# Kernel optimization log

Measured on AMD Instinct MI355X. Metric: run time of the kernel, lower is better.

Reference implementation:

```python
import jax, jax.numpy as jnp
import numpy as np

D_MODEL, N_HEAD, D_HEAD, D_ROPE = 2048, 16, 128, 64
D_KV, D_Q = 512, 1024
THETA = 10000.0


def _cos_sin(seq_len):
    # freqs_cis equivalent: angles [seq_len, d_rope//2]
    inv = 1.0 / (THETA ** (jnp.arange(0, D_ROPE, 2, dtype=jnp.float32) / D_ROPE))
    ang = jnp.arange(seq_len, dtype=jnp.float32)[:, None] * inv[None, :]
    return jnp.cos(ang), jnp.sin(ang)


def _rope(t, cos, sin):
    # t: [b, s, h, d_rope]; rotate interleaved (even, odd) pairs as complex mult
    t1, t2 = t[..., 0::2], t[..., 1::2]
    c = cos[None, :, None, :]
    s = sin[None, :, None, :]
    out = jnp.stack([t1 * c - t2 * s, t1 * s + t2 * c], axis=-1)
    return out.reshape(t.shape)


def setup_inputs() -> dict:
    key = jax.random.key(0)
    ks = jax.random.split(key, 10)
    b, s = 1, 2048
    x = jax.random.normal(ks[0], (b, s, D_MODEL), dtype=jnp.float32)
    # additive causal mask [s, s]
    mask = jnp.where(jnp.tril(jnp.ones((s, s), dtype=bool)), 0.0, -1e9).astype(jnp.float32)
    def w(k, fan_in, fan_out):
        lim = (6.0 / (fan_in + fan_out)) ** 0.5  # xavier_uniform
        return jax.random.uniform(k, (fan_in, fan_out), jnp.float32, -lim, lim)
    return {
        'x': x, 'mask': mask,
        'W_kv_down': w(ks[1], D_MODEL, D_KV),
        'W_k_up':    w(ks[2], D_KV, N_HEAD * D_HEAD),
        'W_v_up':    w(ks[3], D_KV, N_HEAD * D_HEAD),
        'W_q_down':  w(ks[4], D_MODEL, D_Q),
        'W_q_up':    w(ks[5], D_Q, N_HEAD * D_HEAD),
        'W_q_rope':  w(ks[6], D_Q, N_HEAD * D_ROPE),
        'W_k_rope':  w(ks[7], D_MODEL, N_HEAD * D_ROPE),
        'W_out':     w(ks[8], N_HEAD * D_HEAD, D_MODEL),
    }


def reference(x, mask, W_kv_down, W_k_up, W_v_up, W_q_down, W_q_up, W_q_rope, W_k_rope, W_out):
    b, s, _ = x.shape
    cos, sin = _cos_sin(s)
    # low-rank KV path
    down_kv = x @ W_kv_down                                      # [b,s,d_kv]
    k_c = (down_kv @ W_k_up).reshape(b, s, N_HEAD, D_HEAD)
    v   = (down_kv @ W_v_up).reshape(b, s, N_HEAD, D_HEAD)
    # low-rank Q path
    down_q = x @ W_q_down                                        # [b,s,d_q]
    q_c = (down_q @ W_q_up).reshape(b, s, N_HEAD, D_HEAD)
    q_r = (down_q @ W_q_rope).reshape(b, s, N_HEAD, D_ROPE)
    k_r = (x @ W_k_rope).reshape(b, s, N_HEAD, D_ROPE)
    # decoupled RoPE on rope parts only
    q_r = _rope(q_r, cos, sin)
    k_r = _rope(k_r, cos, sin)
    # concat content + rope, heads to dim 1
    q = jnp.concatenate([q_c, q_r], axis=-1).transpose(0, 2, 1, 3)  # [b,h,s,dh+dr]
    k = jnp.concatenate([k_c, k_r], axis=-1).transpose(0, 2, 1, 3)
    vv = v.transpose(0, 2, 1, 3)                                     # [b,h,s,dh]
    scale = 1.0 / jnp.sqrt(jnp.float32(D_HEAD + D_ROPE))
    scores = jnp.einsum('bhqd,bhkd->bhqk', q, k) * scale + mask[None, None]
    probs = jax.nn.softmax(scores.astype(jnp.float32), axis=-1).astype(q.dtype)
    out = jnp.einsum('bhqk,bhkd->bhqd', probs, vv)                   # [b,h,s,dh]
    out = out.transpose(0, 2, 1, 3).reshape(b, s, N_HEAD * D_HEAD)
    return out @ W_out
```

## Files before the change

kernel.cpp:

```cpp
#include <hip/hip_runtime.h>
#include <hip/hip_bf16.h>
#include <math.h>

#define S 2048
#define DM 2048
#define NH 16
#define DH 128
#define DR 64
#define DKV 512
#define DQ 1024
#define DQK 192
#define QSCALE 0.07216878364870323f

typedef __bf16 bf16x8 __attribute__((ext_vector_type(8)));
typedef float f32x4 __attribute__((ext_vector_type(4)));
typedef unsigned short u16;

__device__ inline unsigned int pack2_bf16(float a, float b) {
    __hip_bfloat16 ha = __float2bfloat16(a);
    __hip_bfloat16 hb = __float2bfloat16(b);
    unsigned short ua = *reinterpret_cast<unsigned short*>(&ha);
    unsigned short ub = *reinterpret_cast<unsigned short*>(&hb);
    return (unsigned int)ua | ((unsigned int)ub << 16);
}
__device__ inline u16 f2bf(float v) {
    __hip_bfloat16 hb = __float2bfloat16(v);
    return *reinterpret_cast<u16*>(&hb);
}
__device__ inline void gload_lds16(const void* g, void* l) {
    __builtin_amdgcn_global_load_lds(
        (const __attribute__((address_space(1))) void*)g,
        (__attribute__((address_space(3))) void*)l, 16, 0, 0);
}

__global__ __launch_bounds__(256) void prep_kernel(
    const float* __restrict__ x,
    const float* __restrict__ W0, const float* __restrict__ W1, const float* __restrict__ W2,
    const float* __restrict__ W3, const float* __restrict__ W4, const float* __restrict__ W5,
    const float* __restrict__ W6, const float* __restrict__ W7,
    u16* __restrict__ x_bf,
    u16* __restrict__ D0, u16* __restrict__ D1, u16* __restrict__ D2, u16* __restrict__ D3,
    u16* __restrict__ D4, u16* __restrict__ D5, u16* __restrict__ D6, u16* __restrict__ D7,
    float* __restrict__ cosT, float* __restrict__ sinT) {
    __shared__ u16 tile[64][65];
    const int b = blockIdx.x;
    if (b < 3584) {
        const float* W; u16* D; int N, K, local;
        if (b < 256)       { W = W0; D = D0; N = 512;  K = 2048; local = b; }
        else if (b < 768)  { W = W1; D = D1; N = 1024; K = 2048; local = b - 256; }
        else if (b < 1280) { W = W2; D = D2; N = 1024; K = 2048; local = b - 768; }
        else if (b < 1536) { W = W3; D = D3; N = 2048; K = 512;  local = b - 1280; }
        else if (b < 1792) { W = W4; D = D4; N = 2048; K = 512;  local = b - 1536; }
        else if (b < 2304) { W = W5; D = D5; N = 2048; K = 1024; local = b - 1792; }
        else if (b < 2560) { W = W6; D = D6; N = 1024; K = 1024; local = b - 2304; }
        else               { W = W7; D = D7; N = 2048; K = 2048; local = b - 2560; }
        const int nt = N / 64;
        const int n0 = (local % nt) * 64;
        const int k0 = (local / nt) * 64;
        const int tx = threadIdx.x & 15;
        const int ty = threadIdx.x >> 4;
#pragma unroll
        for (int rep = 0; rep < 4; ++rep) {
            int kk = rep * 16 + ty;
            float4 v = *reinterpret_cast<const float4*>(&W[(size_t)(k0 + kk) * N + n0 + tx * 4]);
            tile[kk][tx * 4 + 0] = f2bf(v.x);
            tile[kk][tx * 4 + 1] = f2bf(v.y);
            tile[kk][tx * 4 + 2] = f2bf(v.z);
            tile[kk][tx * 4 + 3] = f2bf(v.w);
        }
        __syncthreads();
#pragma unroll
        for (int rep = 0; rep < 4; ++rep) {
            int nn = rep * 16 + ty;
            uint2 w;
            w.x = (unsigned int)tile[tx * 4 + 0][nn] | ((unsigned int)tile[tx * 4 + 1][nn] << 16);
            w.y = (unsigned int)tile[tx * 4 + 2][nn] | ((unsigned int)tile[tx * 4 + 3][nn] << 16);
            *reinterpret_cast<uint2*>(&D[(size_t)(n0 + nn) * K + k0 + tx * 4]) = w;
        }
    } else if (b < 7680) {
        int idx = (b - 3584) * 256 + threadIdx.x;
        float4 v = *reinterpret_cast<const float4*>(&x[(size_t)idx * 4]);
        uint2 w;
        w.x = pack2_bf16(v.x, v.y);
        w.y = pack2_bf16(v.z, v.w);
        *reinterpret_cast<uint2*>(&x_bf[(size_t)idx * 4]) = w;
    } else {
        int idx = (b - 7680) * 256 + threadIdx.x;
        int pos = idx / (DR / 2);
        int j   = idx % (DR / 2);
        float inv = __expf(-((float)(2 * j) / (float)DR) * logf(10000.0f));
        float ang = (float)pos * inv;
        cosT[idx] = cosf(ang);
        sinT[idx] = sinf(ang);
    }
}

template <int MODE>
__device__ __forceinline__ void gemm_core(
    u16 (*lds)[6144],
    const u16* __restrict__ A, const u16* __restrict__ BT,
    void* __restrict__ P0v, void* __restrict__ P1v, void* __restrict__ P2v,
    const float* __restrict__ cosT, const float* __restrict__ sinT, int K,
    int bm, int bn) {
    const int tid  = threadIdx.x;
    const int wave = tid >> 6;
    const int lane = tid & 63;
    const int c16  = lane & 15;
    const int g    = lane >> 4;
    const int wm = (wave >> 1) * 32;
    const int wn = (wave & 1) * 64;

    f32x4 acc[2][4];
#pragma unroll
    for (int i = 0; i < 2; ++i)
#pragma unroll
        for (int j = 0; j < 4; ++j) acc[i][j] = f32x4{0.f, 0.f, 0.f, 0.f};

    auto stage = [&](int buf, int k0) {
        {
            int L = tid;
            int rp = L >> 3, e = L & 7, x = e ^ (rp & 7);
            int row = 2 * rp + (x >> 2), kc = x & 3;
            gload_lds16(A + (size_t)(bm + row) * K + k0 + kc * 8, &lds[buf][wave * 512]);
        }
#pragma unroll
        for (int r = 0; r < 2; ++r) {
            int L = r * 256 + tid;
            int rp = L >> 3, e = L & 7, x = e ^ (rp & 7);
            int row = 2 * rp + (x >> 2), kc = x & 3;
            gload_lds16(BT + (size_t)(bn + row) * K + k0 + kc * 8,
                        &lds[buf][2048 + (r * 256 + wave * 64) * 8]);
        }
    };

    const int NT = K / 32;
    stage(0, 0);
    __syncthreads();
    int cur = 0;
    for (int t = 0; t < NT; ++t) {
        if (t + 1 < NT) stage(cur ^ 1, (t + 1) * 32);
        bf16x8 af[2], bfr[4];
#pragma unroll
        for (int i = 0; i < 2; ++i) {
            int row  = wm + i * 16 + c16;
            int slot = ((row >> 1) << 3) + ((((row & 1) << 2) + g) ^ ((row >> 1) & 7));
            af[i] = *reinterpret_cast<const bf16x8*>(&lds[cur][slot * 8]);
        }
#pragma unroll
        for (int j = 0; j < 4; ++j) {
            int row  = wn + j * 16 + c16;
            int slot = ((row >> 1) << 3) + ((((row & 1) << 2) + g) ^ ((row >> 1) & 7));
            bfr[j] = *reinterpret_cast<const bf16x8*>(&lds[cur][2048 + slot * 8]);
        }
#pragma unroll
        for (int i = 0; i < 2; ++i)
#pragma unroll
            for (int j = 0; j < 4; ++j)
                acc[i][j] = __builtin_amdgcn_mfma_f32_16x16x32_bf16(af[i], bfr[j], acc[i][j], 0, 0, 0);
        __syncthreads();
        cur ^= 1;
    }

#pragma unroll
    for (int i = 0; i < 2; ++i)
#pragma unroll
        for (int j = 0; j < 4; ++j) {
            const int mrow = bm + wm + i * 16 + g * 4;
            const int col  = bn + wn + j * 16 + c16;
            if constexpr (MODE == 0) {
                if (col < 512) {
                    u16* down_kv = (u16*)P0v;
#pragma unroll
                    for (int r = 0; r < 4; ++r)
                        down_kv[(size_t)(mrow + r) * DKV + col] = f2bf(acc[i][j][r]);
                } else if (col < 1536) {
                    u16* down_q = (u16*)P1v;
#pragma unroll
                    for (int r = 0; r < 4; ++r)
                        down_q[(size_t)(mrow + r) * DQ + (col - 512)] = f2bf(acc[i][j][r]);
                } else {
                    u16* k_asm = (u16*)P2v;
                    const int cc = col - 1536, h = cc >> 6, rr = cc & 63, jj = rr >> 1;
#pragma unroll
                    for (int r = 0; r < 4; ++r) {
                        int pos = mrow + r;
                        float self = acc[i][j][r];
                        float vp   = __shfl_xor(self, 1);
                        float c = cosT[pos * (DR / 2) + jj];
                        float s = sinT[pos * (DR / 2) + jj];
                        float val = (rr & 1) ? (vp * s + self * c) : (self * c - vp * s);
                        k_asm[((size_t)h * S + pos) * DQK + DH + rr] = f2bf(val);
                    }
                }
            } else if constexpr (MODE == 1) {
                if (col < 2048) {
                    u16* k_asm = (u16*)P0v;
                    const int h = col >> 7, d = col & 127;
#pragma unroll
                    for (int r = 0; r < 4; ++r)
                        k_asm[((size_t)h * S + mrow + r) * DQK + d] = f2bf(acc[i][j][r]);
                } else {
                    u16* vt = (u16*)P1v;
                    const int cc = col - 2048, h = cc >> 7, d = cc & 127;
                    uint2 w;
                    w.x = pack2_bf16(acc[i][j][0], acc[i][j][1]);
                    w.y = pack2_bf16(acc[i][j][2], acc[i][j][3]);
                    *reinterpret_cast<uint2*>(&vt[((size_t)h * DH + d) * S + mrow]) = w;
                }
            } else if constexpr (MODE == 2) {
                u16* q_asm = (u16*)P0v;
                if (col < 2048) {
                    const int h = col >> 7, d = col & 127;
#pragma unroll
                    for (int r = 0; r < 4; ++r)
                        q_asm[((size_t)h * S + mrow + r) * DQK + d] = f2bf(acc[i][j][r] * QSCALE);
                } else {
                    const int cc = col - 2048, h = cc >> 6, rr = cc & 63, jj = rr >> 1;
#pragma unroll
                    for (int r = 0; r < 4; ++r) {
                        int pos = mrow + r;
                        float self = acc[i][j][r];
                        float vp   = __shfl_xor(self, 1);
                        float c = cosT[pos * (DR / 2) + jj];
                        float s = sinT[pos * (DR / 2) + jj];
                        float val = (rr & 1) ? (vp * s + self * c) : (self * c - vp * s);
                        q_asm[((size_t)h * S + pos) * DQK + DH + rr] = f2bf(val * QSCALE);
                    }
                }
            } else {
                float* outp = (float*)P0v;
#pragma unroll
                for (int r = 0; r < 4; ++r)
                    outp[(size_t)(mrow + r) * DM + col] = acc[i][j][r];
            }
        }
}

template <int MODE>
__global__ __launch_bounds__(256) void gemm_fused_kernel(
    const u16* __restrict__ A, const u16* __restrict__ BT,
    void* __restrict__ P0v, void* __restrict__ P1v, void* __restrict__ P2v,
    const float* __restrict__ cosT, const float* __restrict__ sinT, int K) {
    __shared__ u16 lds[2][6144];
    gemm_core<MODE>(lds, A, BT, P0v, P1v, P2v, cosT, sinT, K,
                    blockIdx.y * 64, blockIdx.x * 128);
}

__global__ __launch_bounds__(256) void gemm_g23_kernel(
    const u16* __restrict__ down_kv, const u16* __restrict__ WT2,
    const u16* __restrict__ down_q,  const u16* __restrict__ WT3,
    u16* __restrict__ k_asm, u16* __restrict__ vt, u16* __restrict__ q_asm,
    const float* __restrict__ cosT, const float* __restrict__ sinT) {
    __shared__ u16 lds[2][6144];
    const int b = blockIdx.x;
    if (b < 1024) {
        gemm_core<1>(lds, down_kv, WT2, k_asm, vt, nullptr, cosT, sinT, DKV,
                     (b >> 5) * 64, (b & 31) * 128);
    } else {
        const int l = b - 1024;
        gemm_core<2>(lds, down_q, WT3, q_asm, nullptr, nullptr, cosT, sinT, DQ,
                     (l / 24) * 64, (l % 24) * 128);
    }
}

__global__ __launch_bounds__(512) void attn_mfma_kernel(const u16* __restrict__ q,
                                                        const u16* __restrict__ k,
                                                        const u16* __restrict__ vt,
                                                        u16* __restrict__ outp) {
    const int wgid = blockIdx.x;
    const int xcd  = wgid & 7;
    const int i    = wgid >> 3;
    const int h    = xcd * 2 + (i & 1);
    const int pr   = i >> 1;
    const int qtA  = 31 - pr;
    const int qtB  = pr;

    const int tid  = threadIdx.x;
    const int wave = tid >> 6;
    const int grp  = wave >> 2;
    const int w4   = wave & 3;
    const int lane = tid & 63;
    const int col  = lane & 15;
    const int g    = lane >> 4;

    __shared__ __align__(16) char arena[92160];
    u16* KtG = (u16*)(arena + (grp ? 24576 : 0));
    u16* VtG = (u16*)(arena + 49152 + (grp ? 16384 : 0));
    u16* p_my = (u16*)(arena + 81920 + wave * 1024);
    float2* ml = (float2*)(arena + 90112);
    f32x4* cmb = (f32x4*)(arena);

    const int r7  = col & 7;
    const int pv7 = (col >> 1) & 7;
    const int pvb = (col & 1) << 2;

    auto stage_pair = [&](int buf, int j0E) {
#pragma unroll
        for (int c = 0; c < 5; ++c) {
            int idx = wave + c * 8;
            if (idx < 12) {
                int L = idx * 64 + lane;
                int row = L / 24, rem = L - row * 24;
                int ch  = ((rem >> 3) << 3) + ((rem & 7) ^ (row & 7));
                gload_lds16(k + ((size_t)h * S + j0E + row) * DQK + ch * 8,
                            (u16*)(arena) + buf * 6144 + idx * 512);
            } else if (idx < 20) {
                int s2 = idx - 12;
                int L = s2 * 64 + lane;
                int rp = L >> 3, x = (L & 7) ^ (rp & 7);
                int d  = 2 * rp + (x >> 2), kc = x & 3;
                gload_lds16(vt + ((size_t)h * DH + d) * S + j0E + kc * 8,
                            (u16*)(arena + 49152) + buf * 4096 + s2 * 512);
            } else if (idx < 32) {
                int s2 = idx - 20;
                int L = s2 * 64 + lane;
                int row = L / 24, rem = L - row * 24;
                int ch  = ((rem >> 3) << 3) + ((rem & 7) ^ (row & 7));
                gload_lds16(k + ((size_t)h * S + j0E + 32 + row) * DQK + ch * 8,
                            (u16*)(arena + 24576) + buf * 6144 + s2 * 512);
            } else {
                int s2 = idx - 32;
                int L = s2 * 64 + lane;
                int rp = L >> 3, x = (L & 7) ^ (rp & 7);
                int d  = 2 * rp + (x >> 2), kc = x & 3;
                gload_lds16(vt + ((size_t)h * DH + d) * S + j0E + 32 + kc * 8,
                            (u16*)(arena + 65536) + buf * 4096 + s2 * 512);
            }
        }
    };

    auto phase = [&](int qt) {
        const int q0 = qt * 64;
        const int qw = q0 + w4 * 16;
        const int I  = qt + 1;

        bf16x8 qf[6];
        const u16* qbase = q + ((size_t)h * S + qw + col) * DQK + g * 8;
#pragma unroll
        for (int c = 0; c < 6; ++c) qf[c] = *reinterpret_cast<const bf16x8*>(qbase + c * 32);

        f32x4 acc[8];
#pragma unroll
        for (int c = 0; c < 8; ++c) acc[c] = f32x4{0.f, 0.f, 0.f, 0.f};
        float m_run = -1e30f, l_run = 0.f;

        stage_pair(0, 0);
        __syncthreads();
        for (int tp = 0; tp < I; ++tp) {
            if (tp + 1 < I) stage_pair((tp + 1) & 1, (tp + 1) * 64);
            const int buf = tp & 1;
            const int j0  = tp * 64 + grp * 32;
            const u16* Kc = KtG + buf * 6144;
            const u16* Vc = VtG + buf * 4096;

            f32x4 st[2];
            st[0] = f32x4{0.f, 0.f, 0.f, 0.f};
            st[1] = f32x4{0.f, 0.f, 0.f, 0.f};
#pragma unroll
            for (int tt = 0; tt < 2; ++tt) {
                int rb = (16 * tt + col) * 24;
#pragma unroll
                for (int c = 0; c < 6; ++c) {
                    int ch   = g + 4 * c;
                    int slot = rb + ((ch >> 3) << 3) + ((ch & 7) ^ r7);
                    bf16x8 kf = *reinterpret_cast<const bf16x8*>(Kc + slot * 8);
                    st[tt] = __builtin_amdgcn_mfma_f32_16x16x32_bf16(kf, qf[c], st[tt], 0, 0, 0);
                }
            }
#pragma unroll
            for (int tt = 0; tt < 2; ++tt) {
                if (j0 + 16 * tt + 15 > qw) {
#pragma unroll
                    for (int r = 0; r < 4; ++r) {
                        int key = j0 + 16 * tt + 4 * g + r;
                        st[tt][r] = (key > qw + col) ? -1e30f : st[tt][r];
                    }
                }
            }
            float tmax = fmaxf(fmaxf(fmaxf(st[0][0], st[0][1]), fmaxf(st[0][2], st[0][3])),
                               fmaxf(fmaxf(st[1][0], st[1][1]), fmaxf(st[1][2], st[1][3])));
            tmax = fmaxf(tmax, __shfl_xor(tmax, 16));
            tmax = fmaxf(tmax, __shfl_xor(tmax, 32));
            float m_new;
            if (__all(tmax - m_run <= 8.0f)) {
                m_new = m_run;
            } else {
                m_new = fmaxf(m_run, tmax);
                float r_scale = __expf(m_run - m_new);
                l_run *= r_scale;
#pragma unroll
                for (int c = 0; c < 8; ++c) {
                    acc[c][0] *= r_scale; acc[c][1] *= r_scale;
                    acc[c][2] *= r_scale; acc[c][3] *= r_scale;
                }
                m_run = m_new;
            }
            float m_sub = (m_new <= -1e29f) ? 0.f : m_new;
            float p[8];
            float psum = 0.f;
#pragma unroll
            for (int tt = 0; tt < 2; ++tt)
#pragma unroll
                for (int r = 0; r < 4; ++r) {
                    float pv = __expf(st[tt][r] - m_sub);
                    p[tt * 4 + r] = pv;
                    psum += pv;
                }
            psum += __shfl_xor(psum, 16);
            psum += __shfl_xor(psum, 32);
            l_run += psum;
#pragma unroll
            for (int tt = 0; tt < 2; ++tt) {
                uint2 w;
                w.x = pack2_bf16(p[tt * 4 + 0], p[tt * 4 + 1]);
                w.y = pack2_bf16(p[tt * 4 + 2], p[tt * 4 + 3]);
                int ch   = 2 * tt + (g >> 1);
                int slot = ((col >> 1) << 3) + ((pvb + ch) ^ pv7);
                *reinterpret_cast<uint2*>(p_my + slot * 8 + (g & 1) * 4) = w;
            }
            {
                int slot = ((col >> 1) << 3) + ((pvb + g) ^ pv7);
                bf16x8 pf = *reinterpret_cast<const bf16x8*>(p_my + slot * 8);
#pragma unroll
                for (int c = 0; c < 8; ++c) {
                    int d  = 16 * c + col;
                    int vs = ((d >> 1) << 3) + ((pvb + g) ^ pv7);
                    bf16x8 vf = *reinterpret_cast<const bf16x8*>(Vc + vs * 8);
                    acc[c] = __builtin_amdgcn_mfma_f32_16x16x32_bf16(vf, pf, acc[c], 0, 0, 0);
                }
            }
            __syncthreads();
        }

        if (grp == 1) {
#pragma unroll
            for (int c = 0; c < 8; ++c) cmb[(w4 * 8 + c) * 64 + lane] = acc[c];
            ml[w4 * 64 + lane] = make_float2(m_run, l_run);
        }
        __syncthreads();
        if (grp == 0) {
            float2 mlB = ml[w4 * 64 + lane];
            float m = fmaxf(m_run, mlB.x);
            float sA = __expf(m_run - m);
            float sB = __expf(mlB.x - m);
            float l  = l_run * sA + mlB.y * sB;
            float inv_l = 1.0f / l;
#pragma unroll
            for (int c = 0; c < 8; ++c) {
                f32x4 aB = cmb[(w4 * 8 + c) * 64 + lane];
#pragma unroll
                for (int r = 0; r < 4; ++r) {
                    float v = (acc[c][r] * sA + aB[r] * sB) * inv_l;
                    outp[(size_t)(qw + col) * (NH * DH) + h * DH + 16 * c + 4 * g + r] = f2bf(v);
                }
            }
        }
        __syncthreads();
    };

    phase(qtA);
    phase(qtB);
}

extern "C" void kernel_launch(void* const* d_in, const int* in_sizes, int n_in,
                              void* d_out, int out_size, void* d_ws, size_t ws_size,
                              hipStream_t stream) {
    const float* x         = (const float*)d_in[0];
    const float* W_kv_down = (const float*)d_in[2];
    const float* W_k_up    = (const float*)d_in[3];
    const float* W_v_up    = (const float*)d_in[4];
    const float* W_q_down  = (const float*)d_in[5];
    const float* W_q_up    = (const float*)d_in[6];
    const float* W_q_rope  = (const float*)d_in[7];
    const float* W_k_rope  = (const float*)d_in[8];
    const float* W_out     = (const float*)d_in[9];
    float* out = (float*)d_out;

    float* w = (float*)d_ws;
    float* cosT = w;
    float* sinT = w + (size_t)S * (DR / 2);
    u16* b = (u16*)(w + 2 * (size_t)S * (DR / 2));
    size_t off = 0;
    u16* x_bf    = b + off; off += (size_t)S * DM;
    u16* WT1     = b + off; off += (size_t)2560 * DM;
    u16* WT2     = b + off; off += (size_t)4096 * DKV;
    u16* WT3     = b + off; off += (size_t)3072 * DQ;
    u16* WT4     = b + off; off += (size_t)DM * DM;
    u16* down_kv = b + off; off += (size_t)S * DKV;
    u16* down_q  = b + off; off += (size_t)S * DQ;
    u16* q_asm   = b + off; off += (size_t)NH * S * DQK;
    u16* k_asm   = b + off; off += (size_t)NH * S * DQK;
    u16* vt      = b + off; off += (size_t)NH * DH * S;
    u16* attn_bf = b + off; off += (size_t)S * NH * DH;

    prep_kernel<<<7936, 256, 0, stream>>>(
        x, W_kv_down, W_q_down, W_k_rope, W_k_up, W_v_up, W_q_up, W_q_rope, W_out,
        x_bf,
        WT1, WT1 + (size_t)512 * DM, WT1 + (size_t)1536 * DM,
        WT2, WT2 + (size_t)2048 * DKV,
        WT3, WT3 + (size_t)2048 * DQ, WT4,
        cosT, sinT);

    gemm_fused_kernel<0><<<dim3(2560 / 128, S / 64), 256, 0, stream>>>(
        x_bf, WT1, down_kv, down_q, k_asm, cosT, sinT, DM);

    gemm_g23_kernel<<<1792, 256, 0, stream>>>(
        down_kv, WT2, down_q, WT3, k_asm, vt, q_asm, cosT, sinT);

    attn_mfma_kernel<<<256, 512, 0, stream>>>(q_asm, k_asm, vt, attn_bf);

    gemm_fused_kernel<3><<<dim3(DM / 128, S / 64), 256, 0, stream>>>(
        attn_bf, WT4, out, nullptr, nullptr, cosT, sinT, DM);
}
```

Before: 179.2 us.

## Split K across two wave groups within each GEMM block and reduce via LDS

Each GEMM block grows to 512 threads split into two groups of four waves. Each group accumulates half of the K range in its own double-buffered LDS region, and the partial sums are combined through LDS before the existing epilogue. This raises the number of waves in flight per output tile, to hide global-load latency on the short K loops, and halves the serial K iterations per wave. The cost is twice the LDS per block, an extra reduction pass with a barrier, and possibly fewer resident blocks per CU.

New measurement: 196.9 us. +9.8%, slower.

```diff
diff --git a/kernel.cpp b/kernel.cpp
--- a/kernel.cpp
+++ b/kernel.cpp
@@ -96,19 +96,24 @@
 }
 
 template <int MODE>
-__device__ __forceinline__ void gemm_core(
-    u16 (*lds)[6144],
+__device__ __forceinline__ void gemm_splitk_core(
+    u16 (*lds)[2][6144],
     const u16* __restrict__ A, const u16* __restrict__ BT,
     void* __restrict__ P0v, void* __restrict__ P1v, void* __restrict__ P2v,
     const float* __restrict__ cosT, const float* __restrict__ sinT, int K,
     int bm, int bn) {
     const int tid  = threadIdx.x;
     const int wave = tid >> 6;
+    const int grp  = wave >> 2;
+    const int w4   = wave & 3;
     const int lane = tid & 63;
     const int c16  = lane & 15;
     const int g    = lane >> 4;
-    const int wm = (wave >> 1) * 32;
-    const int wn = (wave & 1) * 64;
+    const int gt   = (w4 << 6) | lane;
+    const int wm = (w4 >> 1) * 32;
+    const int wn = (w4 & 1) * 64;
+    const int Kh    = K >> 1;
+    const int kbase = grp * Kh;
 
     f32x4 acc[2][4];
 #pragma unroll
@@ -117,40 +122,41 @@
         for (int j = 0; j < 4; ++j) acc[i][j] = f32x4{0.f, 0.f, 0.f, 0.f};
 
     auto stage = [&](int buf, int k0) {
+        u16* base = &lds[grp][buf][0];
         {
-            int L = tid;
+            int L = gt;
             int rp = L >> 3, e = L & 7, x = e ^ (rp & 7);
             int row = 2 * rp + (x >> 2), kc = x & 3;
-            gload_lds16(A + (size_t)(bm + row) * K + k0 + kc * 8, &lds[buf][wave * 512]);
+            gload_lds16(A + (size_t)(bm + row) * K + k0 + kc * 8, base + w4 * 512);
         }
 #pragma unroll
         for (int r = 0; r < 2; ++r) {
-            int L = r * 256 + tid;
+            int L = r * 256 + gt;
             int rp = L >> 3, e = L & 7, x = e ^ (rp & 7);
             int row = 2 * rp + (x >> 2), kc = x & 3;
             gload_lds16(BT + (size_t)(bn + row) * K + k0 + kc * 8,
-                        &lds[buf][2048 + (r * 256 + wave * 64) * 8]);
+                        base + 2048 + (r * 256 + w4 * 64) * 8);
         }
     };
 
-    const int NT = K / 32;
-    stage(0, 0);
+    const int NTg = Kh / 32;
+    stage(0, kbase);
     __syncthreads();
     int cur = 0;
-    for (int t = 0; t < NT; ++t) {
-        if (t + 1 < NT) stage(cur ^ 1, (t + 1) * 32);
+    for (int t = 0; t < NTg; ++t) {
+        if (t + 1 < NTg) stage(cur ^ 1, kbase + (t + 1) * 32);
         bf16x8 af[2], bfr[4];
 #pragma unroll
         for (int i = 0; i < 2; ++i) {
             int row  = wm + i * 16 + c16;
             int slot = ((row >> 1) << 3) + ((((row & 1) << 2) + g) ^ ((row >> 1) & 7));
-            af[i] = *reinterpret_cast<const bf16x8*>(&lds[cur][slot * 8]);
+            af[i] = *reinterpret_cast<const bf16x8*>(&lds[grp][cur][slot * 8]);
         }
 #pragma unroll
         for (int j = 0; j < 4; ++j) {
             int row  = wn + j * 16 + c16;
             int slot = ((row >> 1) << 3) + ((((row & 1) << 2) + g) ^ ((row >> 1) & 7));
-            bfr[j] = *reinterpret_cast<const bf16x8*>(&lds[cur][2048 + slot * 8]);
+            bfr[j] = *reinterpret_cast<const bf16x8*>(&lds[grp][cur][2048 + slot * 8]);
         }
 #pragma unroll
         for (int i = 0; i < 2; ++i)
@@ -160,6 +166,24 @@
         __syncthreads();
         cur ^= 1;
     }
+    f32x4* cmb = (f32x4*)lds;
+    if (grp == 1) {
+#pragma unroll
+        for (int i = 0; i < 2; ++i)
+#pragma unroll
+            for (int j = 0; j < 4; ++j)
+                cmb[((w4 << 3) + i * 4 + j) * 64 + lane] = acc[i][j];
+    }
+    __syncthreads();
+    if (grp != 0) return;
+#pragma unroll
+    for (int i = 0; i < 2; ++i)
+#pragma unroll
+        for (int j = 0; j < 4; ++j) {
+            f32x4 o = cmb[((w4 << 3) + i * 4 + j) * 64 + lane];
+            acc[i][j][0] += o[0]; acc[i][j][1] += o[1];
+            acc[i][j][2] += o[2]; acc[i][j][3] += o[3];
+        }
 
 #pragma unroll
     for (int i = 0; i < 2; ++i)
@@ -237,29 +261,29 @@
 }
 
 template <int MODE>
-__global__ __launch_bounds__(256) void gemm_fused_kernel(
+__global__ __launch_bounds__(512) void gemm_splitk_kernel(
     const u16* __restrict__ A, const u16* __restrict__ BT,
     void* __restrict__ P0v, void* __restrict__ P1v, void* __restrict__ P2v,
     const float* __restrict__ cosT, const float* __restrict__ sinT, int K) {
-    __shared__ u16 lds[2][6144];
-    gemm_core<MODE>(lds, A, BT, P0v, P1v, P2v, cosT, sinT, K,
-                    blockIdx.y * 64, blockIdx.x * 128);
-}
-
-__global__ __launch_bounds__(256) void gemm_g23_kernel(
+    __shared__ u16 lds[2][2][6144];
+    gemm_splitk_core<MODE>(lds, A, BT, P0v, P1v, P2v, cosT, sinT, K,
+                           blockIdx.y * 64, blockIdx.x * 128);
+}
+
+__global__ __launch_bounds__(512) void gemm_g23_kernel(
     const u16* __restrict__ down_kv, const u16* __restrict__ WT2,
     const u16* __restrict__ down_q,  const u16* __restrict__ WT3,
     u16* __restrict__ k_asm, u16* __restrict__ vt, u16* __restrict__ q_asm,
     const float* __restrict__ cosT, const float* __restrict__ sinT) {
-    __shared__ u16 lds[2][6144];
+    __shared__ u16 lds[2][2][6144];
     const int b = blockIdx.x;
     if (b < 1024) {
-        gemm_core<1>(lds, down_kv, WT2, k_asm, vt, nullptr, cosT, sinT, DKV,
-                     (b >> 5) * 64, (b & 31) * 128);
+        gemm_splitk_core<1>(lds, down_kv, WT2, k_asm, vt, nullptr, cosT, sinT, DKV,
+                            (b >> 5) * 64, (b & 31) * 128);
     } else {
         const int l = b - 1024;
-        gemm_core<2>(lds, down_q, WT3, q_asm, nullptr, nullptr, cosT, sinT, DQ,
-                     (l / 24) * 64, (l % 24) * 128);
+        gemm_splitk_core<2>(lds, down_q, WT3, q_asm, nullptr, nullptr, cosT, sinT, DQ,
+                            (l / 24) * 64, (l % 24) * 128);
     }
 }
 
@@ -501,14 +525,14 @@
         WT3, WT3 + (size_t)2048 * DQ, WT4,
         cosT, sinT);
 
-    gemm_fused_kernel<0><<<dim3(2560 / 128, S / 64), 256, 0, stream>>>(
+    gemm_splitk_kernel<0><<<dim3(2560 / 128, S / 64), 512, 0, stream>>>(
         x_bf, WT1, down_kv, down_q, k_asm, cosT, sinT, DM);
 
-    gemm_g23_kernel<<<1792, 256, 0, stream>>>(
+    gemm_g23_kernel<<<1792, 512, 0, stream>>>(
         down_kv, WT2, down_q, WT3, k_asm, vt, q_asm, cosT, sinT);
 
     attn_mfma_kernel<<<256, 512, 0, stream>>>(q_asm, k_asm, vt, attn_bf);
 
-    gemm_fused_kernel<3><<<dim3(DM / 128, S / 64), 256, 0, stream>>>(
+    gemm_splitk_kernel<3><<<dim3(DM / 128, S / 64), 512, 0, stream>>>(
         attn_bf, WT4, out, nullptr, nullptr, cosT, sinT, DM);
 }
```
